# Optimization experiments

Measured on AMD Instinct MI355X. Metric: run time of the kernel, lower is better.

Reference implementation:

```python
import jax, jax.numpy as jnp
import numpy as np

N_NODES = 100000
N_EDGES = 1600000
DIM = 128
EPS = 1e-12


def l2_normalize(x):
    # F.normalize(x, p=2, dim=1) with eps=1e-12
    n = jnp.linalg.norm(x, axis=1, keepdims=True)
    return x / jnp.maximum(n, EPS)


def poincare_logmap0(x):
    # logmap at origin, curvature c=1: artanh(||x||) * x / ||x||
    n = jnp.linalg.norm(x, axis=1, keepdims=True)
    n_safe = jnp.maximum(n, EPS)
    n_cl = jnp.clip(n_safe, EPS, 1.0 - 1e-5)
    return jnp.arctanh(n_cl) * x / n_safe


def poincare_expmap0(v):
    # expmap at origin, curvature c=1: tanh(||v||) * v / ||v||
    n = jnp.linalg.norm(v, axis=1, keepdims=True)
    n_safe = jnp.maximum(n, EPS)
    return jnp.tanh(n_safe) * v / n_safe


def mean_aggregate(x, src, dst, n_nodes):
    # DGL copy_u + mean: for each dst node, mean of src-node features over
    # incoming edges; nodes with zero in-degree get zeros.
    msg_sum = jax.ops.segment_sum(x[src], dst, num_segments=n_nodes)  # [N, D]
    deg = jax.ops.segment_sum(jnp.ones_like(dst, dtype=x.dtype), dst,
                              num_segments=n_nodes)  # [N]
    deg = deg[:, None]
    return jnp.where(deg > 0, msg_sum / jnp.maximum(deg, 1.0), 0.0)


def setup_inputs() -> dict:
    key = jax.random.key(0)
    ks = jax.random.split(key, 11)
    e_emb = jax.random.normal(ks[0], (N_NODES, DIM), dtype=jnp.float32)
    b_raw = jax.random.normal(ks[1], (N_NODES, DIM), dtype=jnp.float32)
    # project into open unit Poincare ball (max norm ~0.9)
    b_norm = jnp.linalg.norm(b_raw, axis=1, keepdims=True)
    b_emb = b_raw * (0.9 * jnp.tanh(b_norm) / jnp.maximum(b_norm, EPS))
    s_emb = jax.random.normal(ks[2], (N_NODES, DIM), dtype=jnp.float32)
    src = jax.random.randint(ks[3], (N_EDGES,), 0, N_NODES, dtype=jnp.int32)
    dst = jax.random.randint(ks[4], (N_EDGES,), 0, N_NODES, dtype=jnp.int32)
    scale = 1.0 / np.sqrt(DIM)
    W_e = jax.random.uniform(ks[5], (DIM, DIM), jnp.float32, -scale, scale)
    b_e = jax.random.uniform(ks[6], (DIM,), jnp.float32, -scale, scale)
    W_b = jax.random.uniform(ks[7], (DIM, DIM), jnp.float32, -scale, scale)
    b_b = jax.random.uniform(ks[8], (DIM,), jnp.float32, -scale, scale)
    W_s = jax.random.uniform(ks[9], (DIM, DIM), jnp.float32, -scale, scale)
    b_s = jax.random.uniform(ks[10], (DIM,), jnp.float32, -scale, scale)
    return {"e_emb": e_emb, "b_emb": b_emb, "s_emb": s_emb,
            "W_e": W_e, "b_e": b_e, "W_b": W_b, "b_b": b_b,
            "W_s": W_s, "b_s": b_s, "src": src, "dst": dst}


def reference(e_emb, b_emb, s_emb, W_e, b_e, W_b, b_b, W_s, b_s, src, dst):
    n = e_emb.shape[0]
    # Euclidean branch: aggregate -> linear -> LeakyReLU(0.2)
    e_neigh = mean_aggregate(e_emb, src, dst, n)
    e_lin = e_neigh @ W_e.T + b_e
    e_out = jnp.where(e_lin >= 0, e_lin, 0.2 * e_lin)
    # Poincare branch: logmap0 -> linear -> aggregate -> expmap0
    b_tan = poincare_logmap0(b_emb)
    b_tr = b_tan @ W_b.T + b_b
    b_neigh = mean_aggregate(b_tr, src, dst, n)
    b_out = poincare_expmap0(b_neigh)
    # Spherical branch: normalize -> linear -> aggregate -> normalize
    s_nrm = l2_normalize(s_emb)
    s_tr = s_nrm @ W_s.T + b_s
    s_neigh = mean_aggregate(s_tr, src, dst, n)
    s_out = l2_normalize(s_neigh)
    return (e_out, b_out, s_out)
```

## Files before the change

### kernel.cpp

```cpp
#include <hip/hip_runtime.h>
#include <math.h>

#define N_NODESC 100000
#define N_EDGESC 1600000
#define DIMC 128
#define EPSV 1e-12f

__device__ inline unsigned bf16r(float f) {
    unsigned u = __float_as_uint(f);
    return (u + 0x7FFFu + ((u >> 16) & 1u)) >> 16;
}
__device__ inline unsigned pack2(float lo, float hi) {
    return bf16r(lo) | (bf16r(hi) << 16);
}
__device__ inline float unlo(unsigned u) { return __uint_as_float(u << 16); }
__device__ inline float unhi(unsigned u) { return __uint_as_float(u & 0xFFFF0000u); }

__global__ void pretransform_k(const float* __restrict__ e_emb,
                               const float* __restrict__ b_emb,
                               const float* __restrict__ s_emb,
                               unsigned* __restrict__ tab) {
    int wave = (blockIdx.x * blockDim.x + threadIdx.x) >> 6;
    int lane = threadIdx.x & 63;
    if (wave >= N_NODESC) return;
    float2 ev = ((const float2*)(e_emb + (size_t)wave * DIMC))[lane];
    float2 bv = ((const float2*)(b_emb + (size_t)wave * DIMC))[lane];
    float2 sv = ((const float2*)(s_emb + (size_t)wave * DIMC))[lane];
    float bss = bv.x * bv.x + bv.y * bv.y;
    float sss = sv.x * sv.x + sv.y * sv.y;
    #pragma unroll
    for (int m = 1; m < 64; m <<= 1) {
        bss += __shfl_xor(bss, m, 64);
        sss += __shfl_xor(sss, m, 64);
    }
    float bn  = sqrtf(bss);
    float bns = fmaxf(bn, EPSV);
    float bcl = fminf(fmaxf(bns, EPSV), 1.0f - 1e-5f);
    float bsc = atanhf(bcl) / bns;
    float sn  = sqrtf(sss);
    float ssc = 1.0f / fmaxf(sn, EPSV);
    unsigned* p = tab + (size_t)wave * 192 + lane * 3;
    uint3 v;
    v.x = pack2(ev.x, ev.y);
    v.y = pack2(bv.x * bsc, bv.y * bsc);
    v.z = pack2(sv.x * ssc, sv.y * ssc);
    *(uint3*)p = v;
}

__global__ void hist_k(const int* __restrict__ dst, int* __restrict__ deg) {
    int e = blockIdx.x * 256 + threadIdx.x;
    if (e < N_EDGESC) atomicAdd(&deg[dst[e]], 1);
}

__global__ void scan1_k(const int* __restrict__ deg, int* __restrict__ scanned,
                        int* __restrict__ partials) {
    __shared__ int s[256];
    int t = threadIdx.x;
    int g = blockIdx.x * 256 + t;
    int v = (g < N_NODESC) ? deg[g] : 0;
    s[t] = v;
    __syncthreads();
    for (int off = 1; off < 256; off <<= 1) {
        int x = (t >= off) ? s[t - off] : 0;
        __syncthreads();
        s[t] += x;
        __syncthreads();
    }
    if (g < N_NODESC) scanned[g] = s[t];
    if (t == 255) partials[blockIdx.x] = s[255];
}

__global__ void scan2_k(const int* __restrict__ partials, int* __restrict__ blockoff, int nb) {
    __shared__ int s[512];
    int t = threadIdx.x;
    int v = (t < nb) ? partials[t] : 0;
    s[t] = v;
    __syncthreads();
    for (int off = 1; off < 512; off <<= 1) {
        int x = (t >= off) ? s[t - off] : 0;
        __syncthreads();
        s[t] += x;
        __syncthreads();
    }
    if (t < nb) blockoff[t] = s[t] - v;
}

__global__ void scan3_k(const int* __restrict__ scanned, const int* __restrict__ blockoff,
                        int* __restrict__ offs) {
    int g = blockIdx.x * 256 + threadIdx.x;
    if (g < N_NODESC) offs[g + 1] = scanned[g] + blockoff[blockIdx.x];
    if (g == 0) offs[0] = 0;
}

__global__ void fill_k(const int* __restrict__ src, const int* __restrict__ dst,
                       const int* __restrict__ offs, int* __restrict__ cursor,
                       int* __restrict__ esrc) {
    int e = blockIdx.x * 256 + threadIdx.x;
    if (e < N_EDGESC) {
        int d = dst[e];
        int pos = offs[d] + atomicAdd(&cursor[d], 1);
        esrc[pos] = src[e];
    }
}

__global__ void aggregate_k(const unsigned* __restrict__ tab,
                            const int* __restrict__ offs,
                            const int* __restrict__ esrc,
                            float* __restrict__ out) {
    int wave = (blockIdx.x * blockDim.x + threadIdx.x) >> 6;
    int lane = threadIdx.x & 63;
    if (wave >= N_NODESC) return;
    int beg = offs[wave], end = offs[wave + 1];
    float ae0 = 0.f, ae1 = 0.f, ab0 = 0.f, ab1 = 0.f, as0 = 0.f, as1 = 0.f;
    int j = beg;
    int lo3 = lane * 3;
    for (; j + 1 < end; j += 2) {
        int s0 = esrc[j], s1 = esrc[j + 1];
        uint3 v0 = *(const uint3*)(tab + (size_t)s0 * 192 + lo3);
        uint3 v1 = *(const uint3*)(tab + (size_t)s1 * 192 + lo3);
        ae0 += unlo(v0.x); ae1 += unhi(v0.x);
        ab0 += unlo(v0.y); ab1 += unhi(v0.y);
        as0 += unlo(v0.z); as1 += unhi(v0.z);
        ae0 += unlo(v1.x); ae1 += unhi(v1.x);
        ab0 += unlo(v1.y); ab1 += unhi(v1.y);
        as0 += unlo(v1.z); as1 += unhi(v1.z);
    }
    if (j < end) {
        int s0 = esrc[j];
        uint3 v0 = *(const uint3*)(tab + (size_t)s0 * 192 + lo3);
        ae0 += unlo(v0.x); ae1 += unhi(v0.x);
        ab0 += unlo(v0.y); ab1 += unhi(v0.y);
        as0 += unlo(v0.z); as1 += unhi(v0.z);
    }
    int deg = end - beg;
    float inv = (deg > 0) ? 1.0f / (float)deg : 0.0f;
    ((float2*)(out + (size_t)wave * DIMC))[lane]                           = make_float2(ae0 * inv, ae1 * inv);
    ((float2*)(out + (size_t)(N_NODESC + wave) * DIMC))[lane]              = make_float2(ab0 * inv, ab1 * inv);
    ((float2*)(out + (size_t)(2 * (size_t)N_NODESC + wave) * DIMC))[lane]  = make_float2(as0 * inv, as1 * inv);
}

__global__ __launch_bounds__(256) void gemm_act_k(
    float* __restrict__ out,
    const float* __restrict__ W_e, const float* __restrict__ b_e,
    const float* __restrict__ W_b, const float* __restrict__ b_b,
    const float* __restrict__ W_s, const float* __restrict__ b_s,
    const int* __restrict__ deg) {
    __shared__ float At[64][68];
    __shared__ float Wt[64][132];
    int c = blockIdx.y;
    const float* W    = (c == 0) ? W_e : (c == 1) ? W_b : W_s;
    const float* bias = (c == 0) ? b_e : (c == 1) ? b_b : b_s;
    float* A = out + (size_t)c * N_NODESC * DIMC;
    int m0 = blockIdx.x * 64;
    int tid = threadIdx.x;
    int tx = tid & 31;
    int ty = tid >> 5;
    float acc[8][4] = {};

    for (int h = 0; h < 2; ++h) {
        __syncthreads();
        {
            int m = tid & 63, kq = tid >> 6;
            int row = m0 + m;
            #pragma unroll
            for (int r = 0; r < 4; ++r) {
                int k0 = kq * 16 + r * 4;
                float4 v = make_float4(0.f, 0.f, 0.f, 0.f);
                if (row < N_NODESC)
                    v = *(const float4*)(A + (size_t)row * DIMC + h * 64 + k0);
                At[k0 + 0][m] = v.x; At[k0 + 1][m] = v.y;
                At[k0 + 2][m] = v.z; At[k0 + 3][m] = v.w;
            }
        }
        {
            int j = tid & 127, kh = tid >> 7;
            #pragma unroll
            for (int r = 0; r < 8; ++r) {
                int k0 = kh * 32 + r * 4;
                float4 v = *(const float4*)(W + (size_t)j * DIMC + h * 64 + k0);
                Wt[k0 + 0][j] = v.x; Wt[k0 + 1][j] = v.y;
                Wt[k0 + 2][j] = v.z; Wt[k0 + 3][j] = v.w;
            }
        }
        __syncthreads();
        #pragma unroll 4
        for (int k = 0; k < 64; ++k) {
            float4 w  = *(const float4*)&Wt[k][tx * 4];
            float4 a0 = *(const float4*)&At[k][ty * 8];
            float4 a1 = *(const float4*)&At[k][ty * 8 + 4];
            float am[8] = {a0.x, a0.y, a0.z, a0.w, a1.x, a1.y, a1.z, a1.w};
            #pragma unroll
            for (int r = 0; r < 8; ++r) {
                acc[r][0] += am[r] * w.x;
                acc[r][1] += am[r] * w.y;
                acc[r][2] += am[r] * w.z;
                acc[r][3] += am[r] * w.w;
            }
        }
    }

    float4 bv = *(const float4*)(bias + tx * 4);
    #pragma unroll
    for (int r = 0; r < 8; ++r) {
        int m = ty * 8 + r;
        int row = m0 + m;
        if (row >= N_NODESC) continue;
        float z0 = acc[r][0] + bv.x;
        float z1 = acc[r][1] + bv.y;
        float z2 = acc[r][2] + bv.z;
        float z3 = acc[r][3] + bv.w;
        float4 o;
        if (c == 0) {
            o.x = (z0 >= 0.f) ? z0 : 0.2f * z0;
            o.y = (z1 >= 0.f) ? z1 : 0.2f * z1;
            o.z = (z2 >= 0.f) ? z2 : 0.2f * z2;
            o.w = (z3 >= 0.f) ? z3 : 0.2f * z3;
        } else {
            float ss = z0 * z0 + z1 * z1 + z2 * z2 + z3 * z3;
            #pragma unroll
            for (int mm = 1; mm < 32; mm <<= 1) ss += __shfl_xor(ss, mm, 64);
            float n = sqrtf(ss);
            float scale;
            if (c == 1) {
                float nsafe = fmaxf(n, EPSV);
                scale = tanhf(nsafe) / nsafe;
            } else {
                scale = 1.0f / fmaxf(n, EPSV);
            }
            if (deg[row] <= 0) scale = 0.0f;
            o = make_float4(z0 * scale, z1 * scale, z2 * scale, z3 * scale);
        }
        *(float4*)(A + (size_t)row * DIMC + tx * 4) = o;
    }
}

extern "C" void kernel_launch(void* const* d_in, const int* in_sizes, int n_in,
                              void* d_out, int out_size, void* d_ws, size_t ws_size,
                              hipStream_t stream) {
    const float* e_emb = (const float*)d_in[0];
    const float* b_emb = (const float*)d_in[1];
    const float* s_emb = (const float*)d_in[2];
    const float* W_e   = (const float*)d_in[3];
    const float* b_e   = (const float*)d_in[4];
    const float* W_b   = (const float*)d_in[5];
    const float* b_b   = (const float*)d_in[6];
    const float* W_s   = (const float*)d_in[7];
    const float* b_s   = (const float*)d_in[8];
    const int*   src   = (const int*)d_in[9];
    const int*   dst   = (const int*)d_in[10];
    float* out = (float*)d_out;

    char* w = (char*)d_ws;
    unsigned* tab = (unsigned*)w; w += (size_t)N_NODESC * 192 * sizeof(unsigned);
    int* deg      = (int*)w;   w += (size_t)N_NODESC * sizeof(int);
    int* cursor   = (int*)w;   w += (size_t)N_NODESC * sizeof(int);
    int* scanned  = (int*)w;   w += (size_t)N_NODESC * sizeof(int);
    int* partials = (int*)w;   w += 512 * sizeof(int);
    int* blockoff = (int*)w;   w += 512 * sizeof(int);
    int* offs     = (int*)w;   w += (size_t)(N_NODESC + 1) * sizeof(int);
    w = (char*)(((uintptr_t)w + 255) & ~(uintptr_t)255);
    int* esrc     = (int*)w;   w += (size_t)N_EDGESC * sizeof(int);

    const int nbScan  = (N_NODESC + 255) / 256;
    const int nbEdge  = (N_EDGESC + 255) / 256;
    const int nbNode4 = (N_NODESC + 3) / 4;
    const int nbTile  = (N_NODESC + 63) / 64;

    hipMemsetAsync(deg, 0, (size_t)2 * N_NODESC * sizeof(int), stream);

    pretransform_k<<<nbNode4, 256, 0, stream>>>(e_emb, b_emb, s_emb, tab);
    hist_k<<<nbEdge, 256, 0, stream>>>(dst, deg);
    scan1_k<<<nbScan, 256, 0, stream>>>(deg, scanned, partials);
    scan2_k<<<1, 512, 0, stream>>>(partials, blockoff, nbScan);
    scan3_k<<<nbScan, 256, 0, stream>>>(scanned, blockoff, offs);
    fill_k<<<nbEdge, 256, 0, stream>>>(src, dst, offs, cursor, esrc);
    aggregate_k<<<nbNode4, 256, 0, stream>>>(tab, offs, esrc, out);
    gemm_act_k<<<dim3(nbTile, 3), 256, 0, stream>>>(out, W_e, b_e, W_b, b_b, W_s, b_s, deg);
}
```

Before: 764.1 us.

## Use split-bf16 MFMA for GEMM, fuse histogram into pretransform, unroll aggregate

Replaces the fp32 FMA GEMM epilogue kernel with an MFMA 16x16x32 bf16 kernel that splits A and W into high/low bf16 parts and accumulates three products to retain near-fp32 accuracy. The degree histogram is folded into the pretransform kernel to remove a launch. The aggregate loop is unrolled to four gathered rows per iteration with nontemporal index loads for more memory-level parallelism. The split-bf16 scheme triples MFMA work and adds conversion overhead, and it still carries some precision risk.

After: 640.4 us. 1.19x faster.

```diff
diff --git a/kernel.cpp b/kernel.cpp
--- a/kernel.cpp
+++ b/kernel.cpp
@@ -6,6 +6,9 @@
 #define DIMC 128
 #define EPSV 1e-12f
 
+typedef __attribute__((ext_vector_type(8))) short short8;
+typedef __attribute__((ext_vector_type(4))) float f32x4;
+
 __device__ inline unsigned bf16r(float f) {
     unsigned u = __float_as_uint(f);
     return (u + 0x7FFFu + ((u >> 16) & 1u)) >> 16;
@@ -16,10 +19,22 @@
 __device__ inline float unlo(unsigned u) { return __uint_as_float(u << 16); }
 __device__ inline float unhi(unsigned u) { return __uint_as_float(u & 0xFFFF0000u); }
 
+__device__ inline void bfsplit(float f, unsigned& h, unsigned& l) {
+    h = bf16r(f);
+    float fh = __uint_as_float(h << 16);
+    l = bf16r(f - fh);
+}
+
 __global__ void pretransform_k(const float* __restrict__ e_emb,
                                const float* __restrict__ b_emb,
                                const float* __restrict__ s_emb,
-                               unsigned* __restrict__ tab) {
+                               const int* __restrict__ dst,
+                               unsigned* __restrict__ tab,
+                               int* __restrict__ deg) {
+    {
+        int e = blockIdx.x * 64 + threadIdx.x;
+        if (threadIdx.x < 64 && e < N_EDGESC) atomicAdd(&deg[dst[e]], 1);
+    }
     int wave = (blockIdx.x * blockDim.x + threadIdx.x) >> 6;
     int lane = threadIdx.x & 63;
     if (wave >= N_NODESC) return;
@@ -47,11 +62,6 @@
     *(uint3*)p = v;
 }
 
-__global__ void hist_k(const int* __restrict__ dst, int* __restrict__ deg) {
-    int e = blockIdx.x * 256 + threadIdx.x;
-    if (e < N_EDGESC) atomicAdd(&deg[dst[e]], 1);
-}
-
 __global__ void scan1_k(const int* __restrict__ deg, int* __restrict__ scanned,
                         int* __restrict__ partials) {
     __shared__ int s[256];
@@ -112,21 +122,26 @@
     if (wave >= N_NODESC) return;
     int beg = offs[wave], end = offs[wave + 1];
     float ae0 = 0.f, ae1 = 0.f, ab0 = 0.f, ab1 = 0.f, as0 = 0.f, as1 = 0.f;
+    int lo3 = lane * 3;
     int j = beg;
-    int lo3 = lane * 3;
-    for (; j + 1 < end; j += 2) {
-        int s0 = esrc[j], s1 = esrc[j + 1];
+    for (; j + 3 < end; j += 4) {
+        int s0 = __builtin_nontemporal_load(esrc + j);
+        int s1 = __builtin_nontemporal_load(esrc + j + 1);
+        int s2 = __builtin_nontemporal_load(esrc + j + 2);
+        int s3 = __builtin_nontemporal_load(esrc + j + 3);
         uint3 v0 = *(const uint3*)(tab + (size_t)s0 * 192 + lo3);
         uint3 v1 = *(const uint3*)(tab + (size_t)s1 * 192 + lo3);
-        ae0 += unlo(v0.x); ae1 += unhi(v0.x);
-        ab0 += unlo(v0.y); ab1 += unhi(v0.y);
-        as0 += unlo(v0.z); as1 += unhi(v0.z);
-        ae0 += unlo(v1.x); ae1 += unhi(v1.x);
-        ab0 += unlo(v1.y); ab1 += unhi(v1.y);
-        as0 += unlo(v1.z); as1 += unhi(v1.z);
-    }
-    if (j < end) {
-        int s0 = esrc[j];
+        uint3 v2 = *(const uint3*)(tab + (size_t)s2 * 192 + lo3);
+        uint3 v3 = *(const uint3*)(tab + (size_t)s3 * 192 + lo3);
+        ae0 += (unlo(v0.x) + unlo(v1.x)) + (unlo(v2.x) + unlo(v3.x));
+        ae1 += (unhi(v0.x) + unhi(v1.x)) + (unhi(v2.x) + unhi(v3.x));
+        ab0 += (unlo(v0.y) + unlo(v1.y)) + (unlo(v2.y) + unlo(v3.y));
+        ab1 += (unhi(v0.y) + unhi(v1.y)) + (unhi(v2.y) + unhi(v3.y));
+        as0 += (unlo(v0.z) + unlo(v1.z)) + (unlo(v2.z) + unlo(v3.z));
+        as1 += (unhi(v0.z) + unhi(v1.z)) + (unhi(v2.z) + unhi(v3.z));
+    }
+    for (; j < end; ++j) {
+        int s0 = __builtin_nontemporal_load(esrc + j);
         uint3 v0 = *(const uint3*)(tab + (size_t)s0 * 192 + lo3);
         ae0 += unlo(v0.x); ae1 += unhi(v0.x);
         ab0 += unlo(v0.y); ab1 += unhi(v0.y);
@@ -139,98 +154,121 @@
     ((float2*)(out + (size_t)(2 * (size_t)N_NODESC + wave) * DIMC))[lane]  = make_float2(as0 * inv, as1 * inv);
 }
 
-__global__ __launch_bounds__(256) void gemm_act_k(
+__global__ __launch_bounds__(256, 2) void gemm_mfma_k(
     float* __restrict__ out,
     const float* __restrict__ W_e, const float* __restrict__ b_e,
     const float* __restrict__ W_b, const float* __restrict__ b_b,
     const float* __restrict__ W_s, const float* __restrict__ b_s,
     const int* __restrict__ deg) {
-    __shared__ float At[64][68];
-    __shared__ float Wt[64][132];
+    __shared__ unsigned short Wh[128][72];
+    __shared__ unsigned short Wl[128][72];
     int c = blockIdx.y;
     const float* W    = (c == 0) ? W_e : (c == 1) ? W_b : W_s;
     const float* bias = (c == 0) ? b_e : (c == 1) ? b_b : b_s;
     float* A = out + (size_t)c * N_NODESC * DIMC;
+
+    int tid = threadIdx.x;
+    int wid = tid >> 6, lane = tid & 63;
     int m0 = blockIdx.x * 64;
-    int tid = threadIdx.x;
-    int tx = tid & 31;
-    int ty = tid >> 5;
-    float acc[8][4] = {};
+    int arow = m0 + wid * 16 + (lane & 15);
+    int kb = (lane >> 4) * 8;
+    bool rowok = (arow < N_NODESC);
+    const float* Ap = A + (size_t)arow * DIMC + kb;
+    int colw = lane & 15;
+
+    f32x4 acc[8] = {};
 
     for (int h = 0; h < 2; ++h) {
-        __syncthreads();
-        {
-            int m = tid & 63, kq = tid >> 6;
-            int row = m0 + m;
+        short8 Ah[2], Al[2];
+        #pragma unroll
+        for (int ks = 0; ks < 2; ++ks) {
+            float4 a0 = make_float4(0.f, 0.f, 0.f, 0.f);
+            float4 a1 = a0;
+            if (rowok) {
+                a0 = *(const float4*)(Ap + h * 64 + ks * 32);
+                a1 = *(const float4*)(Ap + h * 64 + ks * 32 + 4);
+            }
+            #define SPLIT8(val, idx) { unsigned hh, ll; bfsplit(val, hh, ll); \
+                Ah[ks][idx] = (short)hh; Al[ks][idx] = (short)ll; }
+            SPLIT8(a0.x, 0) SPLIT8(a0.y, 1) SPLIT8(a0.z, 2) SPLIT8(a0.w, 3)
+            SPLIT8(a1.x, 4) SPLIT8(a1.y, 5) SPLIT8(a1.z, 6) SPLIT8(a1.w, 7)
+            #undef SPLIT8
+        }
+        if (h) __syncthreads();
+        #pragma unroll
+        for (int r = 0; r < 8; ++r) {
+            int flat = (r * 256 + tid) * 4;
+            int n  = flat >> 6;
+            int kk = flat & 63;
+            float4 w4 = *(const float4*)(W + (size_t)n * DIMC + h * 64 + kk);
+            unsigned h0, h1, h2, h3, l0, l1, l2, l3;
+            bfsplit(w4.x, h0, l0); bfsplit(w4.y, h1, l1);
+            bfsplit(w4.z, h2, l2); bfsplit(w4.w, h3, l3);
+            *(uint2*)&Wh[n][kk] = make_uint2(h0 | (h1 << 16), h2 | (h3 << 16));
+            *(uint2*)&Wl[n][kk] = make_uint2(l0 | (l1 << 16), l2 | (l3 << 16));
+        }
+        __syncthreads();
+        #pragma unroll
+        for (int n = 0; n < 8; ++n) {
+            int col = n * 16 + colw;
             #pragma unroll
-            for (int r = 0; r < 4; ++r) {
-                int k0 = kq * 16 + r * 4;
-                float4 v = make_float4(0.f, 0.f, 0.f, 0.f);
-                if (row < N_NODESC)
-                    v = *(const float4*)(A + (size_t)row * DIMC + h * 64 + k0);
-                At[k0 + 0][m] = v.x; At[k0 + 1][m] = v.y;
-                At[k0 + 2][m] = v.z; At[k0 + 3][m] = v.w;
-            }
-        }
-        {
-            int j = tid & 127, kh = tid >> 7;
+            for (int ks = 0; ks < 2; ++ks) {
+                short8 wh = *(const short8*)&Wh[col][ks * 32 + kb];
+                short8 wl = *(const short8*)&Wl[col][ks * 32 + kb];
+                acc[n] = __builtin_amdgcn_mfma_f32_16x16x32_bf16(Ah[ks], wh, acc[n], 0, 0, 0);
+                acc[n] = __builtin_amdgcn_mfma_f32_16x16x32_bf16(Al[ks], wh, acc[n], 0, 0, 0);
+                acc[n] = __builtin_amdgcn_mfma_f32_16x16x32_bf16(Ah[ks], wl, acc[n], 0, 0, 0);
+            }
+        }
+    }
+
+    int r0 = m0 + wid * 16 + (lane >> 4) * 4;
+    float bn[8];
+    #pragma unroll
+    for (int n = 0; n < 8; ++n) bn[n] = bias[n * 16 + colw];
+
+    if (c == 0) {
+        #pragma unroll
+        for (int rg = 0; rg < 4; ++rg) {
+            int row = r0 + rg;
+            if (row >= N_NODESC) continue;
+            float* Ar = A + (size_t)row * DIMC;
             #pragma unroll
-            for (int r = 0; r < 8; ++r) {
-                int k0 = kh * 32 + r * 4;
-                float4 v = *(const float4*)(W + (size_t)j * DIMC + h * 64 + k0);
-                Wt[k0 + 0][j] = v.x; Wt[k0 + 1][j] = v.y;
-                Wt[k0 + 2][j] = v.z; Wt[k0 + 3][j] = v.w;
-            }
-        }
-        __syncthreads();
-        #pragma unroll 4
-        for (int k = 0; k < 64; ++k) {
-            float4 w  = *(const float4*)&Wt[k][tx * 4];
-            float4 a0 = *(const float4*)&At[k][ty * 8];
-            float4 a1 = *(const float4*)&At[k][ty * 8 + 4];
-            float am[8] = {a0.x, a0.y, a0.z, a0.w, a1.x, a1.y, a1.z, a1.w};
+            for (int n = 0; n < 8; ++n) {
+                float z = acc[n][rg] + bn[n];
+                Ar[n * 16 + colw] = (z >= 0.f) ? z : 0.2f * z;
+            }
+        }
+    } else {
+        #pragma unroll
+        for (int rg = 0; rg < 4; ++rg) {
+            float z[8];
+            float ss = 0.f;
             #pragma unroll
-            for (int r = 0; r < 8; ++r) {
-                acc[r][0] += am[r] * w.x;
-                acc[r][1] += am[r] * w.y;
-                acc[r][2] += am[r] * w.z;
-                acc[r][3] += am[r] * w.w;
-            }
-        }
-    }
-
-    float4 bv = *(const float4*)(bias + tx * 4);
-    #pragma unroll
-    for (int r = 0; r < 8; ++r) {
-        int m = ty * 8 + r;
-        int row = m0 + m;
-        if (row >= N_NODESC) continue;
-        float z0 = acc[r][0] + bv.x;
-        float z1 = acc[r][1] + bv.y;
-        float z2 = acc[r][2] + bv.z;
-        float z3 = acc[r][3] + bv.w;
-        float4 o;
-        if (c == 0) {
-            o.x = (z0 >= 0.f) ? z0 : 0.2f * z0;
-            o.y = (z1 >= 0.f) ? z1 : 0.2f * z1;
-            o.z = (z2 >= 0.f) ? z2 : 0.2f * z2;
-            o.w = (z3 >= 0.f) ? z3 : 0.2f * z3;
-        } else {
-            float ss = z0 * z0 + z1 * z1 + z2 * z2 + z3 * z3;
-            #pragma unroll
-            for (int mm = 1; mm < 32; mm <<= 1) ss += __shfl_xor(ss, mm, 64);
-            float n = sqrtf(ss);
+            for (int n = 0; n < 8; ++n) {
+                z[n] = acc[n][rg] + bn[n];
+                ss += z[n] * z[n];
+            }
+            ss += __shfl_xor(ss, 1, 64);
+            ss += __shfl_xor(ss, 2, 64);
+            ss += __shfl_xor(ss, 4, 64);
+            ss += __shfl_xor(ss, 8, 64);
+            float nrm = sqrtf(ss);
             float scale;
             if (c == 1) {
-                float nsafe = fmaxf(n, EPSV);
+                float nsafe = fmaxf(nrm, EPSV);
                 scale = tanhf(nsafe) / nsafe;
             } else {
-                scale = 1.0f / fmaxf(n, EPSV);
-            }
-            if (deg[row] <= 0) scale = 0.0f;
-            o = make_float4(z0 * scale, z1 * scale, z2 * scale, z3 * scale);
-        }
-        *(float4*)(A + (size_t)row * DIMC + tx * 4) = o;
+                scale = 1.0f / fmaxf(nrm, EPSV);
+            }
+            int row = r0 + rg;
+            if (row < N_NODESC) {
+                if (deg[row] <= 0) scale = 0.0f;
+                float* Ar = A + (size_t)row * DIMC;
+                #pragma unroll
+                for (int n = 0; n < 8; ++n) Ar[n * 16 + colw] = z[n] * scale;
+            }
+        }
     }
 }
 
@@ -268,12 +306,11 @@
 
     hipMemsetAsync(deg, 0, (size_t)2 * N_NODESC * sizeof(int), stream);
 
-    pretransform_k<<<nbNode4, 256, 0, stream>>>(e_emb, b_emb, s_emb, tab);
-    hist_k<<<nbEdge, 256, 0, stream>>>(dst, deg);
+    pretransform_k<<<nbNode4, 256, 0, stream>>>(e_emb, b_emb, s_emb, dst, tab, deg);
     scan1_k<<<nbScan, 256, 0, stream>>>(deg, scanned, partials);
     scan2_k<<<1, 512, 0, stream>>>(partials, blockoff, nbScan);
     scan3_k<<<nbScan, 256, 0, stream>>>(scanned, blockoff, offs);
     fill_k<<<nbEdge, 256, 0, stream>>>(src, dst, offs, cursor, esrc);
     aggregate_k<<<nbNode4, 256, 0, stream>>>(tab, offs, esrc, out);
-    gemm_act_k<<<dim3(nbTile, 3), 256, 0, stream>>>(out, W_e, b_e, W_b, b_b, W_s, b_s, deg);
-}
+    gemm_mfma_k<<<dim3(nbTile, 3), 256, 0, stream>>>(out, W_e, b_e, W_b, b_b, W_s, b_s, deg);
+}
```
